# Kernel optimization log

Measured on AMD Instinct MI355X. Metric: run time of the kernel, lower is better.

## Reference

```python
import jax, jax.numpy as jnp
import numpy as np

B, T, C, H = 2, 2048, 1024, 16

def setup_inputs() -> dict:
    key = jax.random.key(0)
    k1, k2, k3 = jax.random.split(key, 3)
    scale = 0.02
    return {
        "x": jax.random.normal(k1, (B, T, C), dtype=jnp.float32),
        "w_attn": jax.random.normal(k2, (C, 3 * C), dtype=jnp.float32) * scale,
        "b_attn": jnp.zeros((3 * C,), dtype=jnp.float32),
        "w_proj": jax.random.normal(k3, (C, C), dtype=jnp.float32) * scale,
        "b_proj": jnp.zeros((C,), dtype=jnp.float32),
    }

def reference(x, w_attn, b_attn, w_proj, b_proj):
    Bx, Tx, Cx = x.shape
    hd = Cx // H  # head dim
    qkv = x @ w_attn + b_attn  # [B,T,3C]
    q, k, v = jnp.split(qkv, 3, axis=-1)
    # [B,H,T,hd]
    q = q.reshape(Bx, Tx, H, hd).transpose(0, 2, 1, 3)
    k = k.reshape(Bx, Tx, H, hd).transpose(0, 2, 1, 3)
    v = v.reshape(Bx, Tx, H, hd).transpose(0, 2, 1, 3)
    att = jnp.einsum('bhqd,bhkd->bhqk', q, k) * (1.0 / jnp.sqrt(jnp.float32(hd)))
    causal = jnp.tril(jnp.ones((Tx, Tx), dtype=bool))  # [T,T]
    att = jnp.where(causal[None, None], att, jnp.float32(-jnp.inf))
    att = jax.nn.softmax(att, axis=-1)
    y = jnp.einsum('bhqk,bhkd->bhqd', att, v)  # [B,H,T,hd]
    y = y.transpose(0, 2, 1, 3).reshape(Bx, Tx, Cx)
    return y @ w_proj + b_proj
```

## Files before the change

### kernel.cpp

```cpp
#include <hip/hip_runtime.h>
#include <hip/hip_bf16.h>
#include <stdint.h>

#define B_SZ 2
#define T_SZ 2048
#define C_SZ 1024
#define H_SZ 16
#define HD   64
#define BH   (B_SZ * H_SZ)
#define M_SZ (B_SZ * T_SZ)
#define N_QKV (3 * C_SZ)

typedef __attribute__((ext_vector_type(8))) __bf16 bf16x8;
typedef __attribute__((ext_vector_type(4))) float f32x4;
typedef __attribute__((ext_vector_type(8))) unsigned short us8;
typedef __attribute__((ext_vector_type(4))) unsigned short us4;
typedef __attribute__((ext_vector_type(4))) unsigned int u32x4;

__device__ __forceinline__ unsigned short f2bf(float f) {
    unsigned int u = __builtin_bit_cast(unsigned int, f);
    u += 0x7fffu + ((u >> 16) & 1u);
    return (unsigned short)(u >> 16);
}

__device__ __forceinline__ void gll16(const unsigned short* g, unsigned short* l) {
    __builtin_amdgcn_global_load_lds(
        (const __attribute__((address_space(1))) unsigned int*)g,
        (__attribute__((address_space(3))) unsigned int*)l, 16, 0, 0);
}

__device__ __forceinline__ void hard_sync() {
    asm volatile("s_waitcnt vmcnt(0) lgkmcnt(0)" ::: "memory");
    __builtin_amdgcn_sched_barrier(0);
    __syncthreads();
}

__global__ __launch_bounds__(256) void k_prep(const float* __restrict__ x,
                                              const float* __restrict__ wa,
                                              const float* __restrict__ wp,
                                              unsigned short* __restrict__ xb,
                                              unsigned short* __restrict__ wta,
                                              unsigned short* __restrict__ wtp) {
    __shared__ float tile[32][33];
    const int tid = threadIdx.x;
    int idx = blockIdx.x;
    if (idx < 2048) {
        const size_t i = ((size_t)idx * 256 + tid) * 8;
        f32x4 a = *(const f32x4*)(x + i);
        f32x4 b = *(const f32x4*)(x + i + 4);
        us8 o;
        #pragma unroll
        for (int j = 0; j < 4; ++j) { o[j] = f2bf(a[j]); o[4 + j] = f2bf(b[j]); }
        *(us8*)(xb + i) = o;
        return;
    }
    const float* in; unsigned short* out; int N;
    if (idx < 5120) { idx -= 2048; in = wa; out = wta; N = N_QKV; }
    else            { idx -= 5120; in = wp; out = wtp; N = C_SZ; }
    const int nx = N / 32;
    const int n0 = (idx % nx) * 32, k0 = (idx / nx) * 32;
    const int tx = tid & 31, ty = tid >> 5;
    #pragma unroll
    for (int j = 0; j < 32; j += 8)
        tile[ty + j][tx] = in[(size_t)(k0 + ty + j) * N + (n0 + tx)];
    __syncthreads();
    #pragma unroll
    for (int j = 0; j < 32; j += 8)
        out[(size_t)(n0 + ty + j) * C_SZ + (k0 + tx)] = f2bf(tile[tx][ty + j]);
}

template <int EPI>
__global__ __launch_bounds__(256) void k_gemm(const unsigned short* __restrict__ A,
                                              const unsigned short* __restrict__ Bt,
                                              const float* __restrict__ bias,
                                              float* __restrict__ Cout,
                                              unsigned short* __restrict__ q_ws,
                                              unsigned short* __restrict__ k_ws,
                                              unsigned short* __restrict__ vT_ws,
                                              int M, int N, int K, int NX) {
    __shared__ __attribute__((aligned(16))) unsigned short Ald[128 * 64];
    __shared__ __attribute__((aligned(16))) unsigned short Bld[128 * 64];
    const int tid = threadIdx.x;
    const int wid = tid >> 6, lane = tid & 63;
    const int wr = wid >> 1, wc = wid & 1;
    const int g = lane >> 4, l15 = lane & 15;
    const int nwg = gridDim.x;
    const int wg = (blockIdx.x & 7) * (nwg >> 3) + (blockIdx.x >> 3);
    const int m0 = (wg / NX) * 128, n0 = (wg % NX) * 128;

    f32x4 acc[4][4];
    #pragma unroll
    for (int i = 0; i < 4; ++i)
        #pragma unroll
        for (int j = 0; j < 4; ++j) acc[i][j] = (f32x4){0.f, 0.f, 0.f, 0.f};

    for (int k0 = 0; k0 < K; k0 += 64) {
        hard_sync();
        #pragma unroll
        for (int i = 0; i < 4; ++i) {
            int c = i * 256 + tid;
            int row = c >> 3;
            int colb = ((c & 7) << 4) ^ ((row & 7) << 4);
            gll16(A  + (size_t)(m0 + row) * K + k0 + (colb >> 1), Ald + i * 2048 + wid * 512);
            gll16(Bt + (size_t)(n0 + row) * K + k0 + (colb >> 1), Bld + i * 2048 + wid * 512);
        }
        hard_sync();

        #pragma unroll
        for (int ks = 0; ks < 2; ++ks) {
            bf16x8 af[4], bfr[4];
            #pragma unroll
            for (int mi = 0; mi < 4; ++mi) {
                int row = wr * 64 + mi * 16 + l15;
                af[mi] = *(const bf16x8*)((const char*)Ald + row * 128 +
                                          ((ks * 64 + g * 16) ^ ((row & 7) << 4)));
            }
            #pragma unroll
            for (int nj = 0; nj < 4; ++nj) {
                int row = wc * 64 + nj * 16 + l15;
                bfr[nj] = *(const bf16x8*)((const char*)Bld + row * 128 +
                                           ((ks * 64 + g * 16) ^ ((row & 7) << 4)));
            }
            #pragma unroll
            for (int mi = 0; mi < 4; ++mi)
                #pragma unroll
                for (int nj = 0; nj < 4; ++nj)
                    acc[mi][nj] = __builtin_amdgcn_mfma_f32_16x16x32_bf16(
                        af[mi], bfr[nj], acc[mi][nj], 0, 0, 0);
        }
    }

    if (EPI == 0) {
        #pragma unroll
        for (int nj = 0; nj < 4; ++nj) {
            int col = n0 + wc * 64 + nj * 16 + l15;
            float bv = bias[col];
            #pragma unroll
            for (int mi = 0; mi < 4; ++mi) {
                int rowb = m0 + wr * 64 + mi * 16 + g * 4;
                #pragma unroll
                for (int r = 0; r < 4; ++r)
                    Cout[(size_t)(rowb + r) * N + col] = acc[mi][nj][r] + bv;
            }
        }
    } else {
        #pragma unroll
        for (int nj = 0; nj < 4; ++nj) {
            int col = n0 + wc * 64 + nj * 16 + l15;
            float bv = bias[col];
            int which = col >> 10;
            int c10 = col & 1023;
            int h = c10 >> 6, d = c10 & 63;
            #pragma unroll
            for (int mi = 0; mi < 4; ++mi) {
                int row0 = m0 + wr * 64 + mi * 16 + g * 4;
                int bb = row0 >> 11, t0 = row0 & 2047;
                if (which == 2) {
                    us4 pk;
                    #pragma unroll
                    for (int r = 0; r < 4; ++r) pk[r] = f2bf(acc[mi][nj][r] + bv);
                    *(us4*)&vT_ws[((size_t)(bb * H_SZ + h) * HD + d) * T_SZ + t0] = pk;
                } else {
                    #pragma unroll
                    for (int r = 0; r < 4; ++r)
                        (which ? k_ws : q_ws)[((size_t)(bb * H_SZ + h) * T_SZ + t0 + r) * HD + d] =
                            f2bf(acc[mi][nj][r] + bv);
                }
            }
        }
    }
}

__global__ __launch_bounds__(512) void k_attn(const unsigned short* __restrict__ q_ws,
                                              const unsigned short* __restrict__ k_ws,
                                              const unsigned short* __restrict__ vT_ws,
                                              unsigned short* __restrict__ y_ws) {
    __shared__ __attribute__((aligned(16))) unsigned short Kbuf[2][8192];
    __shared__ __attribute__((aligned(16))) unsigned short Vbuf[3][8192];
    const int tid = threadIdx.x;
    const int wid = tid >> 6, lane = tid & 63;
    const int g = lane >> 4, l15 = lane & 15;
    const int n = blockIdx.x;
    const int xcd = n & 7, j = (n >> 3) & 7, rk = n >> 6;
    const int bh = xcd + 8 * rk;
    const size_t kv_off = (size_t)bh * T_SZ * HD;
    const unsigned short* Kg = k_ws + kv_off;
    const unsigned short* Vg = vT_ws + (size_t)bh * HD * T_SZ;
    const int b = bh >> 4, h = bh & 15;
    const float SC = 0.125f * 1.44269504f;
    const int qloc = wid * 16 + l15;

    auto stageK = [&](int kv, int buf) {
        #pragma unroll
        for (int i = 0; i < 2; ++i) {
            int c = i * 512 + tid;
            int row = c >> 3;
            int colb = ((c & 7) << 4) ^ ((row & 7) << 4);
            gll16(Kg + (size_t)(kv * 128 + row) * HD + (colb >> 1),
                  &Kbuf[buf][i * 4096 + wid * 512]);
        }
    };
    auto stageV = [&](int kv, int buf) {
        #pragma unroll
        for (int i = 0; i < 2; ++i) {
            int c = i * 512 + tid;
            int row = c >> 4;
            int colb = ((c & 15) << 4) ^ ((row & 15) << 4);
            gll16(Vg + (size_t)row * T_SZ + kv * 128 + (colb >> 1),
                  &Vbuf[buf][i * 4096 + wid * 512]);
        }
    };

    #pragma unroll 1
    for (int phase = 0; phase < 2; ++phase) {
        const int qt = phase ? j : (15 - j);
        const int nkv = qt + 1;

        const int qrow = qt * 128 + wid * 16 + l15;
        bf16x8 aq[2];
        aq[0] = *(const bf16x8*)(q_ws + kv_off + (size_t)qrow * HD + g * 8);
        aq[1] = *(const bf16x8*)(q_ws + kv_off + (size_t)qrow * HD + 32 + g * 8);

        float m_run = -3e38f, l_part = 0.f;
        f32x4 acc[4];
        #pragma unroll
        for (int dt = 0; dt < 4; ++dt) acc[dt] = (f32x4){0.f, 0.f, 0.f, 0.f};
        u32x4 pfA[4], pfB[4];

        auto qk = [&](const char* Kb, f32x4 (&st)[8]) {
            __builtin_amdgcn_s_setprio(1);
            #pragma unroll
            for (int kt = 0; kt < 8; ++kt) {
                f32x4 sv = (f32x4){0.f, 0.f, 0.f, 0.f};
                #pragma unroll
                for (int ks = 0; ks < 2; ++ks) {
                    int row = kt * 16 + l15;
                    bf16x8 ak = *(const bf16x8*)(Kb + row * 128 +
                                                 ((ks * 64 + g * 16) ^ ((row & 7) << 4)));
                    sv = __builtin_amdgcn_mfma_f32_16x16x32_bf16(ak, aq[ks], sv, 0, 0, 0);
                }
                st[kt] = sv;
            }
            __builtin_amdgcn_s_setprio(0);
        };
        auto pv = [&](const char* Vb, const u32x4 (&pf)[4]) {
            __builtin_amdgcn_s_setprio(1);
            #pragma unroll
            for (int ks = 0; ks < 4; ++ks) {
                bf16x8 ap = __builtin_bit_cast(bf16x8, pf[ks]);
                #pragma unroll
                for (int dt = 0; dt < 4; ++dt) {
                    int row = dt * 16 + l15;
                    bf16x8 bv = *(const bf16x8*)(Vb + row * 256 +
                                                 ((ks * 64 + g * 16) ^ ((row & 15) << 4)));
                    acc[dt] = __builtin_amdgcn_mfma_f32_16x16x32_bf16(ap, bv, acc[dt], 0, 0, 0);
                }
            }
            __builtin_amdgcn_s_setprio(0);
        };
        auto softmax = [&](f32x4 (&st)[8], bool diag, u32x4 (&pf)[4]) {
            float t[32];
            #pragma unroll
            for (int kt = 0; kt < 8; ++kt)
                #pragma unroll
                for (int r = 0; r < 4; ++r) t[kt * 4 + r] = st[kt][r];
            if (diag) {
                #pragma unroll
                for (int kt = 0; kt < 8; ++kt)
                    #pragma unroll
                    for (int r = 0; r < 4; ++r)
                        if (kt * 16 + g * 4 + r > qloc) t[kt * 4 + r] = -3e38f;
            }
            float m16v[16];
            #pragma unroll
            for (int i2 = 0; i2 < 16; ++i2) m16v[i2] = fmaxf(t[i2], t[i2 + 16]);
            float m8v[8];
            #pragma unroll
            for (int i2 = 0; i2 < 8; ++i2) m8v[i2] = fmaxf(m16v[i2], m16v[i2 + 8]);
            float m4v[4];
            #pragma unroll
            for (int i2 = 0; i2 < 4; ++i2) m4v[i2] = fmaxf(m8v[i2], m8v[i2 + 4]);
            float mx = fmaxf(fmaxf(m4v[0], m4v[1]), fmaxf(m4v[2], m4v[3]));
            mx = fmaxf(mx, __shfl_xor(mx, 16, 64));
            mx = fmaxf(mx, __shfl_xor(mx, 32, 64));
            float mt = mx * SC;
            if (!__all(mt - m_run <= 8.0f)) {
                float mnew = fmaxf(m_run, mt);
                float alpha = exp2f(m_run - mnew);
                m_run = mnew;
                l_part *= alpha;
                float ao[4];
                #pragma unroll
                for (int r = 0; r < 4; ++r) {
                    int ai = __builtin_amdgcn_ds_bpermute((g * 4 + r) * 4,
                                                          __builtin_bit_cast(int, alpha));
                    ao[r] = __builtin_bit_cast(float, ai);
                }
                #pragma unroll
                for (int dt = 0; dt < 4; ++dt)
                    #pragma unroll
                    for (int r = 0; r < 4; ++r) acc[dt][r] *= ao[r];
            }
            float p[32];
            #pragma unroll
            for (int i2 = 0; i2 < 32; ++i2) p[i2] = exp2f(fmaf(t[i2], SC, -m_run));
            float s16v[16];
            #pragma unroll
            for (int i2 = 0; i2 < 16; ++i2) s16v[i2] = p[i2] + p[i2 + 16];
            float s8v[8];
            #pragma unroll
            for (int i2 = 0; i2 < 8; ++i2) s8v[i2] = s16v[i2] + s16v[i2 + 8];
            float s4v[4];
            #pragma unroll
            for (int i2 = 0; i2 < 4; ++i2) s4v[i2] = s8v[i2] + s8v[i2 + 4];
            l_part += (s4v[0] + s4v[1]) + (s4v[2] + s4v[3]);
            #pragma unroll
            for (int ks = 0; ks < 4; ++ks) {
                unsigned int x0, y0, x1, y1;
                asm("v_cvt_pk_bf16_f32 %0, %1, %2" : "=v"(x0) : "v"(p[8 * ks + 0]), "v"(p[8 * ks + 1]));
                asm("v_cvt_pk_bf16_f32 %0, %1, %2" : "=v"(x1) : "v"(p[8 * ks + 2]), "v"(p[8 * ks + 3]));
                asm("v_cvt_pk_bf16_f32 %0, %1, %2" : "=v"(y0) : "v"(p[8 * ks + 4]), "v"(p[8 * ks + 5]));
                asm("v_cvt_pk_bf16_f32 %0, %1, %2" : "=v"(y1) : "v"(p[8 * ks + 6]), "v"(p[8 * ks + 7]));
                asm("v_permlane32_swap_b32 %0, %1" : "+v"(x0), "+v"(y0));
                asm("v_permlane16_swap_b32 %0, %1" : "+v"(x0), "+v"(y0));
                asm("v_permlane32_swap_b32 %0, %1" : "+v"(x1), "+v"(y1));
                asm("v_permlane16_swap_b32 %0, %1" : "+v"(x1), "+v"(y1));
                pf[ks] = (u32x4){x0, x1, y0, y1};
            }
        };

        hard_sync();
        stageK(0, 0); stageV(0, 0);

        hard_sync();
        if (1 < nkv) { stageK(1, 1); stageV(1, 1); }
        {
            f32x4 st[8];
            qk((const char*)Kbuf[0], st);
            softmax(st, nkv == 1, pfA);
        }
        bool lastA = true;
        for (int i = 1; i < nkv; ) {
            hard_sync();
            if (i + 1 < nkv) { stageK(i + 1, (i + 1) & 1); stageV(i + 1, (i + 1) % 3); }
            {
                f32x4 st[8];
                qk((const char*)Kbuf[i & 1], st);
                pv((const char*)Vbuf[(i - 1) % 3], pfA);
                softmax(st, i == nkv - 1, pfB);
            }
            ++i; lastA = false; if (i == nkv) break;
            hard_sync();
            if (i + 1 < nkv) { stageK(i + 1, (i + 1) & 1); stageV(i + 1, (i + 1) % 3); }
            {
                f32x4 st[8];
                qk((const char*)Kbuf[i & 1], st);
                pv((const char*)Vbuf[(i - 1) % 3], pfB);
                softmax(st, i == nkv - 1, pfA);
            }
            ++i; lastA = true; if (i == nkv) break;
        }
        if (lastA) pv((const char*)Vbuf[(nkv - 1) % 3], pfA);
        else       pv((const char*)Vbuf[(nkv - 1) % 3], pfB);

        float lsum = l_part;
        lsum += __shfl_xor(lsum, 16, 64);
        lsum += __shfl_xor(lsum, 32, 64);
        float lo[4];
        #pragma unroll
        for (int r = 0; r < 4; ++r) {
            int li = __builtin_amdgcn_ds_bpermute((g * 4 + r) * 4,
                                                  __builtin_bit_cast(int, lsum));
            lo[r] = __builtin_bit_cast(float, li);
        }
        #pragma unroll
        for (int r = 0; r < 4; ++r) {
            int tq = qt * 128 + wid * 16 + g * 4 + r;
            float inv = 1.0f / lo[r];
            #pragma unroll
            for (int dt = 0; dt < 4; ++dt)
                y_ws[(size_t)(b * T_SZ + tq) * C_SZ + h * 64 + dt * 16 + l15] =
                    f2bf(acc[dt][r] * inv);
        }
    }
}

extern "C" void kernel_launch(void* const* d_in, const int* in_sizes, int n_in,
                              void* d_out, int out_size, void* d_ws, size_t ws_size,
                              hipStream_t stream) {
    const float* x      = (const float*)d_in[0];
    const float* w_attn = (const float*)d_in[1];
    const float* b_attn = (const float*)d_in[2];
    const float* w_proj = (const float*)d_in[3];
    const float* b_proj = (const float*)d_in[4];
    float* out = (float*)d_out;

    char* ws = (char*)d_ws;
    unsigned short* q_ws  = (unsigned short*)(ws + 0);
    unsigned short* k_ws  = (unsigned short*)(ws + 8388608);
    unsigned short* vT_ws = (unsigned short*)(ws + 16777216);
    unsigned short* wtp   = (unsigned short*)(ws + 25165824);
    unsigned short* xb    = (unsigned short*)(ws + 27262976);
    unsigned short* y_ws  = (unsigned short*)(ws + 27262976);
    unsigned short* wta   = (unsigned short*)(ws + 35651584);

    k_prep<<<dim3(6144), 256, 0, stream>>>(x, w_attn, w_proj, xb, wta, wtp);

    k_gemm<1><<<dim3((N_QKV / 128) * (M_SZ / 128)), 256, 0, stream>>>(
        xb, wta, b_attn, nullptr, q_ws, k_ws, vT_ws, M_SZ, N_QKV, C_SZ, N_QKV / 128);

    k_attn<<<dim3(256), 512, 0, stream>>>(q_ws, k_ws, vT_ws, y_ws);

    k_gemm<0><<<dim3((C_SZ / 128) * (M_SZ / 128)), 256, 0, stream>>>(
        y_ws, wtp, b_proj, out, nullptr, nullptr, nullptr, M_SZ, C_SZ, C_SZ, C_SZ / 128);
}
```

Measured before the change: 110.6 us.

## Split attention into one q-tile per block and shrink V ring to two buffers

The attention kernel now launches 512 blocks, each handling a single (head, q-tile) pair, instead of 256 blocks that each ran a heavy and a light q-tile back to back. The first half of the grid walks q-tiles heavy-first for heads 0-15 and the second half walks them light-first for heads 16-31, so co-resident blocks should roughly pair up long and short work. The V staging ring drops from three buffers to two and V is staged one iteration later, with an added sync before the final PV step. This cuts shared memory per block, so two blocks can share a CU and there are more waves to hide latency. The cost is less prefetch lead for V, and load balance now depends on how the hardware places blocks rather than on explicit pairing.

Result: slower. 132.5 us (+19.9%).

```diff
diff --git a/kernel.cpp b/kernel.cpp
--- a/kernel.cpp
+++ b/kernel.cpp
@@ -176,19 +176,23 @@
                                               const unsigned short* __restrict__ vT_ws,
                                               unsigned short* __restrict__ y_ws) {
     __shared__ __attribute__((aligned(16))) unsigned short Kbuf[2][8192];
-    __shared__ __attribute__((aligned(16))) unsigned short Vbuf[3][8192];
+    __shared__ __attribute__((aligned(16))) unsigned short Vbuf[2][8192];
     const int tid = threadIdx.x;
     const int wid = tid >> 6, lane = tid & 63;
     const int g = lane >> 4, l15 = lane & 15;
     const int n = blockIdx.x;
-    const int xcd = n & 7, j = (n >> 3) & 7, rk = n >> 6;
-    const int bh = xcd + 8 * rk;
+    const int xcd = n & 7;
+    int k = n >> 3;
+    int bh, qt;
+    if (n < 256) { bh = xcd + 8 * (k >> 4);       qt = 15 - (k & 15); }
+    else         { k -= 32; bh = 16 + xcd + 8 * (k >> 4); qt = k & 15; }
     const size_t kv_off = (size_t)bh * T_SZ * HD;
     const unsigned short* Kg = k_ws + kv_off;
     const unsigned short* Vg = vT_ws + (size_t)bh * HD * T_SZ;
     const int b = bh >> 4, h = bh & 15;
     const float SC = 0.125f * 1.44269504f;
     const int qloc = wid * 16 + l15;
+    const int nkv = qt + 1;
 
     auto stageK = [&](int kv, int buf) {
         #pragma unroll
@@ -211,177 +215,173 @@
         }
     };
 
-    #pragma unroll 1
-    for (int phase = 0; phase < 2; ++phase) {
-        const int qt = phase ? j : (15 - j);
-        const int nkv = qt + 1;
-
-        const int qrow = qt * 128 + wid * 16 + l15;
-        bf16x8 aq[2];
-        aq[0] = *(const bf16x8*)(q_ws + kv_off + (size_t)qrow * HD + g * 8);
-        aq[1] = *(const bf16x8*)(q_ws + kv_off + (size_t)qrow * HD + 32 + g * 8);
-
-        float m_run = -3e38f, l_part = 0.f;
-        f32x4 acc[4];
-        #pragma unroll
-        for (int dt = 0; dt < 4; ++dt) acc[dt] = (f32x4){0.f, 0.f, 0.f, 0.f};
-        u32x4 pfA[4], pfB[4];
-
-        auto qk = [&](const char* Kb, f32x4 (&st)[8]) {
-            __builtin_amdgcn_s_setprio(1);
-            #pragma unroll
-            for (int kt = 0; kt < 8; ++kt) {
-                f32x4 sv = (f32x4){0.f, 0.f, 0.f, 0.f};
-                #pragma unroll
-                for (int ks = 0; ks < 2; ++ks) {
-                    int row = kt * 16 + l15;
-                    bf16x8 ak = *(const bf16x8*)(Kb + row * 128 +
-                                                 ((ks * 64 + g * 16) ^ ((row & 7) << 4)));
-                    sv = __builtin_amdgcn_mfma_f32_16x16x32_bf16(ak, aq[ks], sv, 0, 0, 0);
-                }
-                st[kt] = sv;
-            }
-            __builtin_amdgcn_s_setprio(0);
-        };
-        auto pv = [&](const char* Vb, const u32x4 (&pf)[4]) {
-            __builtin_amdgcn_s_setprio(1);
-            #pragma unroll
-            for (int ks = 0; ks < 4; ++ks) {
-                bf16x8 ap = __builtin_bit_cast(bf16x8, pf[ks]);
-                #pragma unroll
-                for (int dt = 0; dt < 4; ++dt) {
-                    int row = dt * 16 + l15;
-                    bf16x8 bv = *(const bf16x8*)(Vb + row * 256 +
-                                                 ((ks * 64 + g * 16) ^ ((row & 15) << 4)));
-                    acc[dt] = __builtin_amdgcn_mfma_f32_16x16x32_bf16(ap, bv, acc[dt], 0, 0, 0);
-                }
-            }
-            __builtin_amdgcn_s_setprio(0);
-        };
-        auto softmax = [&](f32x4 (&st)[8], bool diag, u32x4 (&pf)[4]) {
-            float t[32];
+    const int qrow = qt * 128 + wid * 16 + l15;
+    bf16x8 aq[2];
+    aq[0] = *(const bf16x8*)(q_ws + kv_off + (size_t)qrow * HD + g * 8);
+    aq[1] = *(const bf16x8*)(q_ws + kv_off + (size_t)qrow * HD + 32 + g * 8);
+
+    float m_run = -3e38f, l_part = 0.f;
+    f32x4 acc[4];
+    #pragma unroll
+    for (int dt = 0; dt < 4; ++dt) acc[dt] = (f32x4){0.f, 0.f, 0.f, 0.f};
+    u32x4 pfA[4], pfB[4];
+
+    auto qk = [&](const char* Kb, f32x4 (&st)[8]) {
+        __builtin_amdgcn_s_setprio(1);
+        #pragma unroll
+        for (int kt = 0; kt < 8; ++kt) {
+            f32x4 sv = (f32x4){0.f, 0.f, 0.f, 0.f};
+            #pragma unroll
+            for (int ks = 0; ks < 2; ++ks) {
+                int row = kt * 16 + l15;
+                bf16x8 ak = *(const bf16x8*)(Kb + row * 128 +
+                                             ((ks * 64 + g * 16) ^ ((row & 7) << 4)));
+                sv = __builtin_amdgcn_mfma_f32_16x16x32_bf16(ak, aq[ks], sv, 0, 0, 0);
+            }
+            st[kt] = sv;
+        }
+        __builtin_amdgcn_s_setprio(0);
+    };
+    auto pv = [&](const char* Vb, const u32x4 (&pf)[4]) {
+        __builtin_amdgcn_s_setprio(1);
+        #pragma unroll
+        for (int ks = 0; ks < 4; ++ks) {
+            bf16x8 ap = __builtin_bit_cast(bf16x8, pf[ks]);
+            #pragma unroll
+            for (int dt = 0; dt < 4; ++dt) {
+                int row = dt * 16 + l15;
+                bf16x8 bv = *(const bf16x8*)(Vb + row * 256 +
+                                             ((ks * 64 + g * 16) ^ ((row & 15) << 4)));
+                acc[dt] = __builtin_amdgcn_mfma_f32_16x16x32_bf16(ap, bv, acc[dt], 0, 0, 0);
+            }
+        }
+        __builtin_amdgcn_s_setprio(0);
+    };
+    auto softmax = [&](f32x4 (&st)[8], bool diag, u32x4 (&pf)[4]) {
+        float t[32];
+        #pragma unroll
+        for (int kt = 0; kt < 8; ++kt)
+            #pragma unroll
+            for (int r = 0; r < 4; ++r) t[kt * 4 + r] = st[kt][r];
+        if (diag) {
             #pragma unroll
             for (int kt = 0; kt < 8; ++kt)
                 #pragma unroll
-                for (int r = 0; r < 4; ++r) t[kt * 4 + r] = st[kt][r];
-            if (diag) {
+                for (int r = 0; r < 4; ++r)
+                    if (kt * 16 + g * 4 + r > qloc) t[kt * 4 + r] = -3e38f;
+        }
+        float m16v[16];
+        #pragma unroll
+        for (int i2 = 0; i2 < 16; ++i2) m16v[i2] = fmaxf(t[i2], t[i2 + 16]);
+        float m8v[8];
+        #pragma unroll
+        for (int i2 = 0; i2 < 8; ++i2) m8v[i2] = fmaxf(m16v[i2], m16v[i2 + 8]);
+        float m4v[4];
+        #pragma unroll
+        for (int i2 = 0; i2 < 4; ++i2) m4v[i2] = fmaxf(m8v[i2], m8v[i2 + 4]);
+        float mx = fmaxf(fmaxf(m4v[0], m4v[1]), fmaxf(m4v[2], m4v[3]));
+        mx = fmaxf(mx, __shfl_xor(mx, 16, 64));
+        mx = fmaxf(mx, __shfl_xor(mx, 32, 64));
+        float mt = mx * SC;
+        if (!__all(mt - m_run <= 8.0f)) {
+            float mnew = fmaxf(m_run, mt);
+            float alpha = exp2f(m_run - mnew);
+            m_run = mnew;
+            l_part *= alpha;
+            float ao[4];
+            #pragma unroll
+            for (int r = 0; r < 4; ++r) {
+                int ai = __builtin_amdgcn_ds_bpermute((g * 4 + r) * 4,
+                                                      __builtin_bit_cast(int, alpha));
+                ao[r] = __builtin_bit_cast(float, ai);
+            }
+            #pragma unroll
+            for (int dt = 0; dt < 4; ++dt)
                 #pragma unroll
-                for (int kt = 0; kt < 8; ++kt)
-                    #pragma unroll
-                    for (int r = 0; r < 4; ++r)
-                        if (kt * 16 + g * 4 + r > qloc) t[kt * 4 + r] = -3e38f;
-            }
-            float m16v[16];
-            #pragma unroll
-            for (int i2 = 0; i2 < 16; ++i2) m16v[i2] = fmaxf(t[i2], t[i2 + 16]);
-            float m8v[8];
-            #pragma unroll
-            for (int i2 = 0; i2 < 8; ++i2) m8v[i2] = fmaxf(m16v[i2], m16v[i2 + 8]);
-            float m4v[4];
-            #pragma unroll
-            for (int i2 = 0; i2 < 4; ++i2) m4v[i2] = fmaxf(m8v[i2], m8v[i2 + 4]);
-            float mx = fmaxf(fmaxf(m4v[0], m4v[1]), fmaxf(m4v[2], m4v[3]));
-            mx = fmaxf(mx, __shfl_xor(mx, 16, 64));
-            mx = fmaxf(mx, __shfl_xor(mx, 32, 64));
-            float mt = mx * SC;
-            if (!__all(mt - m_run <= 8.0f)) {
-                float mnew = fmaxf(m_run, mt);
-                float alpha = exp2f(m_run - mnew);
-                m_run = mnew;
-                l_part *= alpha;
-                float ao[4];
-                #pragma unroll
-                for (int r = 0; r < 4; ++r) {
-                    int ai = __builtin_amdgcn_ds_bpermute((g * 4 + r) * 4,
-                                                          __builtin_bit_cast(int, alpha));
-                    ao[r] = __builtin_bit_cast(float, ai);
-                }
-                #pragma unroll
-                for (int dt = 0; dt < 4; ++dt)
-                    #pragma unroll
-                    for (int r = 0; r < 4; ++r) acc[dt][r] *= ao[r];
-            }
-            float p[32];
-            #pragma unroll
-            for (int i2 = 0; i2 < 32; ++i2) p[i2] = exp2f(fmaf(t[i2], SC, -m_run));
-            float s16v[16];
-            #pragma unroll
-            for (int i2 = 0; i2 < 16; ++i2) s16v[i2] = p[i2] + p[i2 + 16];
-            float s8v[8];
-            #pragma unroll
-            for (int i2 = 0; i2 < 8; ++i2) s8v[i2] = s16v[i2] + s16v[i2 + 8];
-            float s4v[4];
-            #pragma unroll
-            for (int i2 = 0; i2 < 4; ++i2) s4v[i2] = s8v[i2] + s8v[i2 + 4];
-            l_part += (s4v[0] + s4v[1]) + (s4v[2] + s4v[3]);
-            #pragma unroll
-            for (int ks = 0; ks < 4; ++ks) {
-                unsigned int x0, y0, x1, y1;
-                asm("v_cvt_pk_bf16_f32 %0, %1, %2" : "=v"(x0) : "v"(p[8 * ks + 0]), "v"(p[8 * ks + 1]));
-                asm("v_cvt_pk_bf16_f32 %0, %1, %2" : "=v"(x1) : "v"(p[8 * ks + 2]), "v"(p[8 * ks + 3]));
-                asm("v_cvt_pk_bf16_f32 %0, %1, %2" : "=v"(y0) : "v"(p[8 * ks + 4]), "v"(p[8 * ks + 5]));
-                asm("v_cvt_pk_bf16_f32 %0, %1, %2" : "=v"(y1) : "v"(p[8 * ks + 6]), "v"(p[8 * ks + 7]));
-                asm("v_permlane32_swap_b32 %0, %1" : "+v"(x0), "+v"(y0));
-                asm("v_permlane16_swap_b32 %0, %1" : "+v"(x0), "+v"(y0));
-                asm("v_permlane32_swap_b32 %0, %1" : "+v"(x1), "+v"(y1));
-                asm("v_permlane16_swap_b32 %0, %1" : "+v"(x1), "+v"(y1));
-                pf[ks] = (u32x4){x0, x1, y0, y1};
-            }
-        };
-
+                for (int r = 0; r < 4; ++r) acc[dt][r] *= ao[r];
+        }
+        float p[32];
+        #pragma unroll
+        for (int i2 = 0; i2 < 32; ++i2) p[i2] = exp2f(fmaf(t[i2], SC, -m_run));
+        float s16v[16];
+        #pragma unroll
+        for (int i2 = 0; i2 < 16; ++i2) s16v[i2] = p[i2] + p[i2 + 16];
+        float s8v[8];
+        #pragma unroll
+        for (int i2 = 0; i2 < 8; ++i2) s8v[i2] = s16v[i2] + s16v[i2 + 8];
+        float s4v[4];
+        #pragma unroll
+        for (int i2 = 0; i2 < 4; ++i2) s4v[i2] = s8v[i2] + s8v[i2 + 4];
+        l_part += (s4v[0] + s4v[1]) + (s4v[2] + s4v[3]);
+        #pragma unroll
+        for (int ks = 0; ks < 4; ++ks) {
+            unsigned int x0, y0, x1, y1;
+            asm("v_cvt_pk_bf16_f32 %0, %1, %2" : "=v"(x0) : "v"(p[8 * ks + 0]), "v"(p[8 * ks + 1]));
+            asm("v_cvt_pk_bf16_f32 %0, %1, %2" : "=v"(x1) : "v"(p[8 * ks + 2]), "v"(p[8 * ks + 3]));
+            asm("v_cvt_pk_bf16_f32 %0, %1, %2" : "=v"(y0) : "v"(p[8 * ks + 4]), "v"(p[8 * ks + 5]));
+            asm("v_cvt_pk_bf16_f32 %0, %1, %2" : "=v"(y1) : "v"(p[8 * ks + 6]), "v"(p[8 * ks + 7]));
+            asm("v_permlane32_swap_b32 %0, %1" : "+v"(x0), "+v"(y0));
+            asm("v_permlane16_swap_b32 %0, %1" : "+v"(x0), "+v"(y0));
+            asm("v_permlane32_swap_b32 %0, %1" : "+v"(x1), "+v"(y1));
+            asm("v_permlane16_swap_b32 %0, %1" : "+v"(x1), "+v"(y1));
+            pf[ks] = (u32x4){x0, x1, y0, y1};
+        }
+    };
+
+    stageK(0, 0);
+    hard_sync();
+    if (1 < nkv) stageK(1, 1);
+    stageV(0, 0);
+    {
+        f32x4 st[8];
+        qk((const char*)Kbuf[0], st);
+        softmax(st, nkv == 1, pfA);
+    }
+    bool lastA = true;
+    for (int i = 1; i < nkv; ) {
         hard_sync();
-        stageK(0, 0); stageV(0, 0);
-
-        hard_sync();
-        if (1 < nkv) { stageK(1, 1); stageV(1, 1); }
+        if (i + 1 < nkv) stageK(i + 1, (i + 1) & 1);
+        stageV(i, i & 1);
         {
             f32x4 st[8];
-            qk((const char*)Kbuf[0], st);
-            softmax(st, nkv == 1, pfA);
-        }
-        bool lastA = true;
-        for (int i = 1; i < nkv; ) {
-            hard_sync();
-            if (i + 1 < nkv) { stageK(i + 1, (i + 1) & 1); stageV(i + 1, (i + 1) % 3); }
-            {
-                f32x4 st[8];
-                qk((const char*)Kbuf[i & 1], st);
-                pv((const char*)Vbuf[(i - 1) % 3], pfA);
-                softmax(st, i == nkv - 1, pfB);
-            }
-            ++i; lastA = false; if (i == nkv) break;
-            hard_sync();
-            if (i + 1 < nkv) { stageK(i + 1, (i + 1) & 1); stageV(i + 1, (i + 1) % 3); }
-            {
-                f32x4 st[8];
-                qk((const char*)Kbuf[i & 1], st);
-                pv((const char*)Vbuf[(i - 1) % 3], pfB);
-                softmax(st, i == nkv - 1, pfA);
-            }
-            ++i; lastA = true; if (i == nkv) break;
-        }
-        if (lastA) pv((const char*)Vbuf[(nkv - 1) % 3], pfA);
-        else       pv((const char*)Vbuf[(nkv - 1) % 3], pfB);
-
-        float lsum = l_part;
-        lsum += __shfl_xor(lsum, 16, 64);
-        lsum += __shfl_xor(lsum, 32, 64);
-        float lo[4];
-        #pragma unroll
-        for (int r = 0; r < 4; ++r) {
-            int li = __builtin_amdgcn_ds_bpermute((g * 4 + r) * 4,
-                                                  __builtin_bit_cast(int, lsum));
-            lo[r] = __builtin_bit_cast(float, li);
-        }
-        #pragma unroll
-        for (int r = 0; r < 4; ++r) {
-            int tq = qt * 128 + wid * 16 + g * 4 + r;
-            float inv = 1.0f / lo[r];
-            #pragma unroll
-            for (int dt = 0; dt < 4; ++dt)
-                y_ws[(size_t)(b * T_SZ + tq) * C_SZ + h * 64 + dt * 16 + l15] =
-                    f2bf(acc[dt][r] * inv);
-        }
+            qk((const char*)Kbuf[i & 1], st);
+            pv((const char*)Vbuf[(i - 1) & 1], pfA);
+            softmax(st, i == nkv - 1, pfB);
+        }
+        ++i; lastA = false; if (i == nkv) break;
+        hard_sync();
+        if (i + 1 < nkv) stageK(i + 1, (i + 1) & 1);
+        stageV(i, i & 1);
+        {
+            f32x4 st[8];
+            qk((const char*)Kbuf[i & 1], st);
+            pv((const char*)Vbuf[(i - 1) & 1], pfB);
+            softmax(st, i == nkv - 1, pfA);
+        }
+        ++i; lastA = true;
+    }
+    hard_sync();
+    if (lastA) pv((const char*)Vbuf[(nkv - 1) & 1], pfA);
+    else       pv((const char*)Vbuf[(nkv - 1) & 1], pfB);
+
+    float lsum = l_part;
+    lsum += __shfl_xor(lsum, 16, 64);
+    lsum += __shfl_xor(lsum, 32, 64);
+    float lo[4];
+    #pragma unroll
+    for (int r = 0; r < 4; ++r) {
+        int li = __builtin_amdgcn_ds_bpermute((g * 4 + r) * 4,
+                                              __builtin_bit_cast(int, lsum));
+        lo[r] = __builtin_bit_cast(float, li);
+    }
+    #pragma unroll
+    for (int r = 0; r < 4; ++r) {
+        int tq = qt * 128 + wid * 16 + g * 4 + r;
+        float inv = 1.0f / lo[r];
+        #pragma unroll
+        for (int dt = 0; dt < 4; ++dt)
+            y_ws[(size_t)(b * T_SZ + tq) * C_SZ + h * 64 + dt * 16 + l15] =
+                f2bf(acc[dt][r] * inv);
     }
 }
 
@@ -409,7 +409,7 @@
     k_gemm<1><<<dim3((N_QKV / 128) * (M_SZ / 128)), 256, 0, stream>>>(
         xb, wta, b_attn, nullptr, q_ws, k_ws, vT_ws, M_SZ, N_QKV, C_SZ, N_QKV / 128);
 
-    k_attn<<<dim3(256), 512, 0, stream>>>(q_ws, k_ws, vT_ws, y_ws);
+    k_attn<<<dim3(512), 512, 0, stream>>>(q_ws, k_ws, vT_ws, y_ws);
 
     k_gemm<0><<<dim3((C_SZ / 128) * (M_SZ / 128)), 256, 0, stream>>>(
         y_ws, wtp, b_proj, out, nullptr, nullptr, nullptr, M_SZ, C_SZ, C_SZ, C_SZ / 128);
```
